# Performance work log

Measured on AMD Instinct MI355X. Metric: run time of the kernel, lower is better.

Reference implementation:

```python
import jax, jax.numpy as jnp
import numpy as np

B, N, D, H = 2, 2048, 1024, 16
HD = D // H  # head_dim = 64
LN_EPS = 1e-5


def rotate_half(x):
    # x: [..., HD] with interleaved pairs -> (-x2, x1) interleaved back
    x = x.reshape(*x.shape[:-1], HD // 2, 2)
    x1, x2 = x[..., 0], x[..., 1]
    return jnp.stack((-x2, x1), axis=-1).reshape(*x.shape[:-2], HD)


def setup_inputs() -> dict:
    key = jax.random.key(0)
    ks = jax.random.split(key, 12)
    s = 0.02
    return {
        "descriptor": jax.random.normal(ks[0], (B, N, D), dtype=jnp.float32),
        "encoding": jax.random.normal(ks[1], (2, B, H, N, HD), dtype=jnp.float32),
        "w_qkv": s * jax.random.normal(ks[2], (3 * D, D), dtype=jnp.float32),
        "b_qkv": jnp.zeros((3 * D,), dtype=jnp.float32),
        "w_out": s * jax.random.normal(ks[3], (D, D), dtype=jnp.float32),
        "b_out": jnp.zeros((D,), dtype=jnp.float32),
        "w_ffn1": s * jax.random.normal(ks[4], (2 * D, 2 * D), dtype=jnp.float32),
        "b_ffn1": jnp.zeros((2 * D,), dtype=jnp.float32),
        "ln_g": jnp.ones((2 * D,), dtype=jnp.float32),
        "ln_b": jnp.zeros((2 * D,), dtype=jnp.float32),
        "w_ffn2": s * jax.random.normal(ks[5], (D, 2 * D), dtype=jnp.float32),
        "b_ffn2": jnp.zeros((D,), dtype=jnp.float32),
    }


def reference(descriptor, encoding, w_qkv, b_qkv, w_out, b_out,
              w_ffn1, b_ffn1, ln_g, ln_b, w_ffn2, b_ffn2):
    # fused QKV projection; last dim laid out as (H, HD, 3) like the torch code
    qkv = descriptor @ w_qkv.T + b_qkv                      # [B, N, 3D]
    qkv = qkv.reshape(B, N, H, HD, 3).transpose(0, 2, 1, 3, 4)  # [B, H, N, HD, 3]
    q, k, v = qkv[..., 0], qkv[..., 1], qkv[..., 2]

    # cached rotary embedding
    q = q * encoding[0] + rotate_half(q) * encoding[1]
    k = k * encoding[0] + rotate_half(k) * encoding[1]

    # scaled dot-product attention (no mask)
    scale = 1.0 / jnp.sqrt(jnp.asarray(HD, dtype=q.dtype))
    scores = jnp.einsum('bhqd,bhkd->bhqk', q, k) * scale    # [B, H, N, N]
    attn = jax.nn.softmax(scores, axis=-1)
    context = jnp.einsum('bhqk,bhkd->bhqd', attn, v)        # [B, H, N, HD]

    message = context.transpose(0, 2, 1, 3).reshape(B, N, D) @ w_out.T + b_out

    # concat-FFN: Linear -> LayerNorm -> GELU -> Linear
    h = jnp.concatenate([descriptor, message], axis=-1) @ w_ffn1.T + b_ffn1  # [B, N, 2D]
    mu = jnp.mean(h, axis=-1, keepdims=True)
    var = jnp.mean(jnp.square(h - mu), axis=-1, keepdims=True)
    h = (h - mu) * jax.lax.rsqrt(var + LN_EPS) * ln_g + ln_b
    h = jax.nn.gelu(h, approximate=False)
    return descriptor + h @ w_ffn2.T + b_ffn2
```

## Files before the change

kernel.cpp:

```cpp
#include <hip/hip_runtime.h>
#include <hip/hip_bf16.h>
#include <stdint.h>
#include <stddef.h>

#define B_   2
#define N_   2048
#define D_   1024
#define H_   16
#define HD_  64
#define BH_  (B_ * H_)
#define M_   (B_ * N_)

typedef short bf16x8 __attribute__((ext_vector_type(8)));
typedef float f32x4  __attribute__((ext_vector_type(4)));

static __device__ __forceinline__ unsigned short f2bf(float f) {
    union { float f; unsigned u; } c; c.f = f;
    unsigned r = (c.u + 0x7FFFu + ((c.u >> 16) & 1u)) >> 16;
    return (unsigned short)r;
}
static __device__ __forceinline__ float bf2f(unsigned short u) {
    union { unsigned u; float f; } c; c.u = ((unsigned)u) << 16; return c.f;
}

#define GLDS16(g, l)                                                                     \
    __builtin_amdgcn_global_load_lds((const __attribute__((address_space(1))) void*)(g), \
                                     (__attribute__((address_space(3))) void*)(l), 16, 0, 0)

__global__ __launch_bounds__(256) void k_cast(const float* __restrict__ in,
                                              unsigned short* __restrict__ out, int n) {
    int i = (blockIdx.x * 256 + threadIdx.x) * 4;
    if (i >= n) return;
    float4 v = *(const float4*)(in + i);
    ushort4 o;
    o.x = f2bf(v.x); o.y = f2bf(v.y); o.z = f2bf(v.z); o.w = f2bf(v.w);
    *(ushort4*)(out + i) = o;
}

__global__ __launch_bounds__(256) void k_cast_desc(const float* __restrict__ in,
                                                   unsigned short* __restrict__ cat) {
    int i = (blockIdx.x * 256 + threadIdx.x) * 4;
    float4 v = *(const float4*)(in + i);
    int row = i >> 10, col = i & 1023;
    ushort4 o;
    o.x = f2bf(v.x); o.y = f2bf(v.y); o.z = f2bf(v.z); o.w = f2bf(v.w);
    *(ushort4*)(cat + (size_t)row * 2048 + col) = o;
}

template <int EPI>
__global__ __launch_bounds__(256) void k_gemm(const unsigned short* __restrict__ A, int lda,
                                              const unsigned short* __restrict__ Bm, int ldb,
                                              void* __restrict__ Cv, int ldc,
                                              const float* __restrict__ bias,
                                              const float* __restrict__ resid, int ldr,
                                              unsigned short* __restrict__ qd,
                                              unsigned short* __restrict__ kd,
                                              unsigned short* __restrict__ vd,
                                              int K) {
    __shared__ unsigned short As[128 * 64];
    __shared__ unsigned short Bs[128 * 64];
    const int tid  = threadIdx.x;
    const int wave = tid >> 6, lane = tid & 63;
    const int wr = wave >> 1, wc = wave & 1;
    const int brow = blockIdx.y * 128, bcol = blockIdx.x * 128;

    const int srow = (lane >> 3);
    const int scol = (lane & 7) * 8;
    const int frow = lane & 15;
    const int fk   = (lane >> 4) * 8;

    f32x4 acc[4][4] = {};

    for (int kt = 0; kt < K; kt += 64) {
        __syncthreads();
#pragma unroll
        for (int j = 0; j < 4; ++j) {
            int r = wave * 32 + j * 8 + srow;
            GLDS16(A  + (size_t)(brow + r) * lda + kt + scol, (char*)As + wave * 4096 + j * 1024);
            GLDS16(Bm + (size_t)(bcol + r) * ldb + kt + scol, (char*)Bs + wave * 4096 + j * 1024);
        }
        __syncthreads();
#pragma unroll
        for (int ks = 0; ks < 2; ++ks) {
            bf16x8 a[4], b[4];
#pragma unroll
            for (int m = 0; m < 4; ++m)
                a[m] = *(const bf16x8*)(As + (wr * 64 + m * 16 + frow) * 64 + ks * 32 + fk);
#pragma unroll
            for (int n = 0; n < 4; ++n)
                b[n] = *(const bf16x8*)(Bs + (wc * 64 + n * 16 + frow) * 64 + ks * 32 + fk);
#pragma unroll
            for (int m = 0; m < 4; ++m)
#pragma unroll
                for (int n = 0; n < 4; ++n)
                    acc[m][n] = __builtin_amdgcn_mfma_f32_16x16x32_bf16(a[m], b[n], acc[m][n], 0, 0, 0);
        }
    }

    const int orow = (lane >> 4) * 4;
#pragma unroll
    for (int m = 0; m < 4; ++m) {
        int row0 = brow + wr * 64 + m * 16 + orow;
#pragma unroll
        for (int n = 0; n < 4; ++n) {
            int col = bcol + wc * 64 + n * 16 + frow;
            float bs = bias[col];
#pragma unroll
            for (int r = 0; r < 4; ++r) {
                float v = acc[m][n][r] + bs;
                if (EPI == 3) {
                    int row = row0 + r;
                    int bb = row >> 11, nr = row & (N_ - 1);
                    int h = col / 192;
                    int rem = col - h * 192;
                    int d = rem / 3;
                    int c = rem - d * 3;
                    unsigned short* dst = (c == 0) ? qd : (c == 1) ? kd : vd;
                    dst[(((size_t)(bb * H_ + h)) * N_ + nr) * 64 + d] = f2bf(v);
                } else if (EPI == 2) {
                    v += resid[(size_t)(row0 + r) * ldr + col];
                    ((float*)Cv)[(size_t)(row0 + r) * ldc + col] = v;
                } else {
                    ((unsigned short*)Cv)[(size_t)(row0 + r) * ldc + col] = f2bf(v);
                }
            }
        }
    }
}

__global__ __launch_bounds__(256) void k_rope_ip(unsigned short* __restrict__ Qb,
                                                 unsigned short* __restrict__ Kb,
                                                 const float* __restrict__ enc) {
    int idx = blockIdx.x * 256 + threadIdx.x;
    int i  = idx & 31;
    int n  = (idx >> 5) & (N_ - 1);
    int bh = idx >> 16;
    size_t eoff = ((size_t)bh * N_ + n) * 64 + i * 2;
    float2 e0 = *(const float2*)(enc + eoff);
    float2 e1 = *(const float2*)(enc + (size_t)BH_ * N_ * 64 + eoff);
    ushort2 qp = *(const ushort2*)(Qb + eoff);
    ushort2 kp = *(const ushort2*)(Kb + eoff);
    float q1 = bf2f(qp.x), q2 = bf2f(qp.y);
    float k1 = bf2f(kp.x), k2 = bf2f(kp.y);
    ushort2 qo, ko;
    qo.x = f2bf(q1 * e0.x - q2 * e1.x);
    qo.y = f2bf(q2 * e0.y + q1 * e1.y);
    ko.x = f2bf(k1 * e0.x - k2 * e1.x);
    ko.y = f2bf(k2 * e0.y + k1 * e1.y);
    *(ushort2*)(Qb + eoff) = qo;
    *(ushort2*)(Kb + eoff) = ko;
}

__global__ __launch_bounds__(256) void k_transpose_v(const unsigned short* __restrict__ Vb,
                                                     unsigned short* __restrict__ Vt) {
    __shared__ unsigned short t[64][72];
    int bh = blockIdx.y, n0 = blockIdx.x * 64;
    int tid = threadIdx.x;
    int r  = tid >> 2;
    int c0 = (tid & 3) * 16;
    const unsigned short* src = Vb + ((size_t)bh * N_ + n0 + r) * 64 + c0;
    *(bf16x8*)(&t[r][c0])     = *(const bf16x8*)(src);
    *(bf16x8*)(&t[r][c0 + 8]) = *(const bf16x8*)(src + 8);
    __syncthreads();
    int d  = tid >> 2;
    int nc = (tid & 3) * 16;
    bf16x8 o0, o1;
#pragma unroll
    for (int j = 0; j < 8; ++j) { o0[j] = (short)t[nc + j][d]; o1[j] = (short)t[nc + 8 + j][d]; }
    unsigned short* dst = Vt + ((size_t)bh * 64 + d) * N_ + n0 + nc;
    *(bf16x8*)(dst)     = o0;
    *(bf16x8*)(dst + 8) = o1;
}

__global__ __launch_bounds__(256) void k_attn(const unsigned short* __restrict__ Qb,
                                              const unsigned short* __restrict__ Kb,
                                              const unsigned short* __restrict__ Vt,
                                              unsigned short* __restrict__ Ctx) {
    __shared__ unsigned short Ks[64 * 64];
    __shared__ unsigned short Vs[64 * 64];
    __shared__ unsigned short Ps[4][16 * 64];
    int bh = blockIdx.y;
    int b = bh >> 4, h = bh & 15;
    int q0 = blockIdx.x * 64;
    int tid = threadIdx.x, wave = tid >> 6, lane = tid & 63;
    int frow = lane & 15, fk = (lane >> 4) * 8, g = lane >> 4;

    const unsigned short* qptr = Qb + ((size_t)bh * N_ + q0 + wave * 16 + frow) * 64;
    bf16x8 qf[2];
    qf[0] = *(const bf16x8*)(qptr + fk);
    qf[1] = *(const bf16x8*)(qptr + 32 + fk);

    float mrow[4] = {-INFINITY, -INFINITY, -INFINITY, -INFINITY};
    float lrow[4] = {0.f, 0.f, 0.f, 0.f};
    f32x4 accO[4] = {};

    for (int kt = 0; kt < N_; kt += 64) {
        __syncthreads();
#pragma unroll
        for (int j = 0; j < 2; ++j) {
            int r = wave * 16 + j * 8 + (lane >> 3);
            GLDS16(Kb + ((size_t)bh * N_ + kt + r) * 64 + (lane & 7) * 8,
                   (char*)Ks + wave * 2048 + j * 1024);
            GLDS16(Vt + ((size_t)bh * 64 + r) * N_ + kt + (lane & 7) * 8,
                   (char*)Vs + wave * 2048 + j * 1024);
        }
        __syncthreads();

        f32x4 s[4];
#pragma unroll
        for (int kc = 0; kc < 4; ++kc) {
            f32x4 a = {};
#pragma unroll
            for (int ks = 0; ks < 2; ++ks) {
                bf16x8 kfr = *(const bf16x8*)(Ks + (kc * 16 + frow) * 64 + ks * 32 + fk);
                a = __builtin_amdgcn_mfma_f32_16x16x32_bf16(qf[ks], kfr, a, 0, 0, 0);
            }
            s[kc] = a * 0.125f;
        }

        float scl[4];
#pragma unroll
        for (int r = 0; r < 4; ++r) {
            float mx = fmaxf(fmaxf(s[0][r], s[1][r]), fmaxf(s[2][r], s[3][r]));
            mx = fmaxf(mx, __shfl_xor(mx, 1));
            mx = fmaxf(mx, __shfl_xor(mx, 2));
            mx = fmaxf(mx, __shfl_xor(mx, 4));
            mx = fmaxf(mx, __shfl_xor(mx, 8));
            float mn = fmaxf(mrow[r], mx);
            float sc = __expf(mrow[r] - mn);
            mrow[r] = mn;
            float ps = 0.f;
#pragma unroll
            for (int kc = 0; kc < 4; ++kc) {
                float p = __expf(s[kc][r] - mn);
                s[kc][r] = p;
                ps += p;
            }
            ps += __shfl_xor(ps, 1);
            ps += __shfl_xor(ps, 2);
            ps += __shfl_xor(ps, 4);
            ps += __shfl_xor(ps, 8);
            lrow[r] = lrow[r] * sc + ps;
            scl[r] = sc;
        }
#pragma unroll
        for (int df = 0; df < 4; ++df)
#pragma unroll
            for (int r = 0; r < 4; ++r) accO[df][r] *= scl[r];

#pragma unroll
        for (int kc = 0; kc < 4; ++kc)
#pragma unroll
            for (int r = 0; r < 4; ++r)
                Ps[wave][(g * 4 + r) * 64 + kc * 16 + frow] = f2bf(s[kc][r]);
        asm volatile("s_waitcnt lgkmcnt(0)" ::: "memory");
        __builtin_amdgcn_sched_barrier(0);

#pragma unroll
        for (int ks = 0; ks < 2; ++ks) {
            bf16x8 pa = *(const bf16x8*)(&Ps[wave][frow * 64 + ks * 32 + fk]);
#pragma unroll
            for (int df = 0; df < 4; ++df) {
                bf16x8 vf = *(const bf16x8*)(Vs + (df * 16 + frow) * 64 + ks * 32 + fk);
                accO[df] = __builtin_amdgcn_mfma_f32_16x16x32_bf16(pa, vf, accO[df], 0, 0, 0);
            }
        }
    }

#pragma unroll
    for (int df = 0; df < 4; ++df)
#pragma unroll
        for (int r = 0; r < 4; ++r) {
            int q = q0 + wave * 16 + g * 4 + r;
            float v = accO[df][r] / lrow[r];
            Ctx[((size_t)(b * N_ + q)) * D_ + h * 64 + df * 16 + frow] = f2bf(v);
        }
}

__global__ __launch_bounds__(256) void k_ln_gelu(const unsigned short* __restrict__ hsrc,
                                                 const float* __restrict__ gma,
                                                 const float* __restrict__ bta,
                                                 unsigned short* __restrict__ out) {
    __shared__ float red[2][4];
    int row = blockIdx.x, tid = threadIdx.x;
    const unsigned short* hr = hsrc + (size_t)row * 2048 + tid * 8;
    bf16x8 hv = *(const bf16x8*)(hr);
    float xs[8];
    float s = 0.f, q = 0.f;
#pragma unroll
    for (int j = 0; j < 8; ++j) {
        float x = bf2f((unsigned short)hv[j]);
        xs[j] = x; s += x; q += x * x;
    }
#pragma unroll
    for (int off = 1; off < 64; off <<= 1) {
        s += __shfl_xor(s, off);
        q += __shfl_xor(q, off);
    }
    int wave = tid >> 6;
    if ((tid & 63) == 0) { red[0][wave] = s; red[1][wave] = q; }
    __syncthreads();
    s = red[0][0] + red[0][1] + red[0][2] + red[0][3];
    q = red[1][0] + red[1][1] + red[1][2] + red[1][3];
    float mu   = s * (1.f / 2048.f);
    float var  = q * (1.f / 2048.f) - mu * mu;
    float rstd = rsqrtf(var + 1e-5f);
    int c = tid * 8;
#pragma unroll
    for (int j = 0; j < 8; ++j) {
        float x = (xs[j] - mu) * rstd * gma[c + j] + bta[c + j];
        float y = 0.5f * x * (1.f + erff(x * 0.70710678118654752f));
        out[(size_t)row * 2048 + c + j] = f2bf(y);
    }
}

extern "C" void kernel_launch(void* const* d_in, const int* in_sizes, int n_in,
                              void* d_out, int out_size, void* d_ws, size_t ws_size,
                              hipStream_t stream) {
    const float* descriptor = (const float*)d_in[0];
    const float* encoding   = (const float*)d_in[1];
    const float* w_qkv      = (const float*)d_in[2];
    const float* b_qkv      = (const float*)d_in[3];
    const float* w_out      = (const float*)d_in[4];
    const float* b_out      = (const float*)d_in[5];
    const float* w_ffn1     = (const float*)d_in[6];
    const float* b_ffn1     = (const float*)d_in[7];
    const float* ln_g       = (const float*)d_in[8];
    const float* ln_b       = (const float*)d_in[9];
    const float* w_ffn2     = (const float*)d_in[10];
    const float* b_ffn2     = (const float*)d_in[11];
    float* out = (float*)d_out;

    char* ws = (char*)d_ws;
    unsigned short* wffn1_b = (unsigned short*)(ws);
    unsigned short* wffn2_b = (unsigned short*)(ws + ((size_t)8  << 20));
    unsigned short* wout_b  = (unsigned short*)(ws + ((size_t)12 << 20));
    unsigned short* cat     = (unsigned short*)(ws + ((size_t)14 << 20));
    unsigned short* Qb      = (unsigned short*)(ws + ((size_t)30 << 20));
    unsigned short* Kb      = (unsigned short*)(ws + ((size_t)38 << 20));
    unsigned short* Vb      = (unsigned short*)(ws + ((size_t)46 << 20));
    unsigned short* wqkv_b  = (unsigned short*)(ws + ((size_t)54 << 20));
    unsigned short* Vt      = (unsigned short*)(ws + ((size_t)54 << 20));
    unsigned short* msg     = (unsigned short*)(ws + ((size_t)46 << 20));
    unsigned short* hbuf    = (unsigned short*)(ws + ((size_t)30 << 20));
    unsigned short* h2      = (unsigned short*)(ws + ((size_t)14 << 20));

    k_cast_desc<<<4096, 256, 0, stream>>>(descriptor, cat);
    k_cast<<<3072, 256, 0, stream>>>(w_qkv, wqkv_b, 3145728);
    k_cast<<<1024, 256, 0, stream>>>(w_out, wout_b, 1048576);
    k_cast<<<4096, 256, 0, stream>>>(w_ffn1, wffn1_b, 4194304);
    k_cast<<<2048, 256, 0, stream>>>(w_ffn2, wffn2_b, 2097152);

    k_gemm<3><<<dim3(24, 32), 256, 0, stream>>>(cat, 2048, wqkv_b, 1024, nullptr, 0,
                                                b_qkv, nullptr, 0, Qb, Kb, Vb, 1024);
    k_rope_ip<<<8192, 256, 0, stream>>>(Qb, Kb, encoding);
    k_transpose_v<<<dim3(32, 32), 256, 0, stream>>>(Vb, Vt);
    k_attn<<<dim3(32, 32), 256, 0, stream>>>(Qb, Kb, Vt, msg);
    k_gemm<1><<<dim3(8, 32), 256, 0, stream>>>(msg, 1024, wout_b, 1024, cat + 1024, 2048,
                                               b_out, nullptr, 0, nullptr, nullptr, nullptr, 1024);
    k_gemm<1><<<dim3(16, 32), 256, 0, stream>>>(cat, 2048, wffn1_b, 2048, hbuf, 2048,
                                                b_ffn1, nullptr, 0, nullptr, nullptr, nullptr, 2048);
    k_ln_gelu<<<4096, 256, 0, stream>>>(hbuf, ln_g, ln_b, h2);
    k_gemm<2><<<dim3(8, 32), 256, 0, stream>>>(h2, 2048, wffn2_b, 2048, out, 1024,
                                               b_ffn2, descriptor, 1024, nullptr, nullptr, nullptr, 2048);
}
```

Baseline: 521.5 us.

## Double-buffer attention K/V tiles, swizzle LDS, fold scale into exp2, merge weight casts

The attention kernel now double-buffers its K/V tiles in LDS, prefetching the next tile while computing the current one, which removes one barrier per iteration. LDS reads and writes use an XOR swizzle to avoid bank conflicts. The softmax scale times log2(e) is folded into Q during RoPE so the kernel can use exp2f and skip the per-score multiply. The change also adds wave priority hints, remaps blocks across heads, uses a reciprocal for the final normalization, and merges the four weight cast launches into one. Together these raise LDS usage and mix several unrelated changes.

```diff
diff --git a/kernel.cpp b/kernel.cpp
--- a/kernel.cpp
+++ b/kernel.cpp
@@ -27,14 +27,26 @@
     __builtin_amdgcn_global_load_lds((const __attribute__((address_space(1))) void*)(g), \
                                      (__attribute__((address_space(3))) void*)(l), 16, 0, 0)
 
-__global__ __launch_bounds__(256) void k_cast(const float* __restrict__ in,
-                                              unsigned short* __restrict__ out, int n) {
-    int i = (blockIdx.x * 256 + threadIdx.x) * 4;
-    if (i >= n) return;
-    float4 v = *(const float4*)(in + i);
+#define QSCALE 0.18033688011112042f
+
+__global__ __launch_bounds__(256) void k_cast_w4(const float* __restrict__ s0,
+                                                 const float* __restrict__ s1,
+                                                 const float* __restrict__ s2,
+                                                 const float* __restrict__ s3,
+                                                 unsigned short* __restrict__ d0,
+                                                 unsigned short* __restrict__ d1,
+                                                 unsigned short* __restrict__ d2,
+                                                 unsigned short* __restrict__ d3) {
+    int i = blockIdx.x * 256 + threadIdx.x;
+    const float* s; unsigned short* d; int off;
+    if (i < 786432)              { s = s0; d = d0; off = i; }
+    else if (i < 1048576)        { s = s1; d = d1; off = i - 786432; }
+    else if (i < 2097152)        { s = s2; d = d2; off = i - 1048576; }
+    else                         { s = s3; d = d3; off = i - 2097152; }
+    float4 v = *(const float4*)(s + (size_t)off * 4);
     ushort4 o;
     o.x = f2bf(v.x); o.y = f2bf(v.y); o.z = f2bf(v.z); o.w = f2bf(v.w);
-    *(ushort4*)(out + i) = o;
+    *(ushort4*)(d + (size_t)off * 4) = o;
 }
 
 __global__ __launch_bounds__(256) void k_cast_desc(const float* __restrict__ in,
@@ -143,8 +155,8 @@
     float q1 = bf2f(qp.x), q2 = bf2f(qp.y);
     float k1 = bf2f(kp.x), k2 = bf2f(kp.y);
     ushort2 qo, ko;
-    qo.x = f2bf(q1 * e0.x - q2 * e1.x);
-    qo.y = f2bf(q2 * e0.y + q1 * e1.y);
+    qo.x = f2bf((q1 * e0.x - q2 * e1.x) * QSCALE);
+    qo.y = f2bf((q2 * e0.y + q1 * e1.y) * QSCALE);
     ko.x = f2bf(k1 * e0.x - k2 * e1.x);
     ko.y = f2bf(k2 * e0.y + k1 * e1.y);
     *(ushort2*)(Qb + eoff) = qo;
@@ -176,14 +188,36 @@
                                               const unsigned short* __restrict__ Kb,
                                               const unsigned short* __restrict__ Vt,
                                               unsigned short* __restrict__ Ctx) {
-    __shared__ unsigned short Ks[64 * 64];
-    __shared__ unsigned short Vs[64 * 64];
+    __shared__ unsigned short Ks[2][64 * 64];
+    __shared__ unsigned short Vs[2][64 * 64];
     __shared__ unsigned short Ps[4][16 * 64];
-    int bh = blockIdx.y;
+
+    int lin = blockIdx.x + 32 * blockIdx.y;
+    int ixc = lin >> 3;
+    int bh  = (lin & 7) * 4 + (ixc >> 5);
+    int q0  = (ixc & 31) * 64;
     int b = bh >> 4, h = bh & 15;
-    int q0 = blockIdx.x * 64;
     int tid = threadIdx.x, wave = tid >> 6, lane = tid & 63;
     int frow = lane & 15, fk = (lane >> 4) * 8, g = lane >> 4;
+    int f7x8 = (frow & 7) * 8;
+
+    int srow = lane >> 3;
+    int scol = ((lane & 7) ^ srow) * 8;
+
+    const unsigned short* Kbh = Kb + (size_t)bh * N_ * 64;
+    const unsigned short* Vbh = Vt + (size_t)bh * 64 * N_;
+
+#define ATTN_STAGE(bufi, kt)                                                           \
+    do {                                                                               \
+        _Pragma("unroll")                                                              \
+        for (int j = 0; j < 2; ++j) {                                                  \
+            int rr = wave * 16 + j * 8 + srow;                                         \
+            GLDS16(Kbh + (size_t)((kt) + rr) * 64 + scol,                              \
+                   (char*)Ks[bufi] + wave * 2048 + j * 1024);                          \
+            GLDS16(Vbh + (size_t)rr * N_ + (kt) + scol,                                \
+                   (char*)Vs[bufi] + wave * 2048 + j * 1024);                          \
+        }                                                                              \
+    } while (0)
 
     const unsigned short* qptr = Qb + ((size_t)bh * N_ + q0 + wave * 16 + frow) * 64;
     bf16x8 qf[2];
@@ -194,29 +228,26 @@
     float lrow[4] = {0.f, 0.f, 0.f, 0.f};
     f32x4 accO[4] = {};
 
-    for (int kt = 0; kt < N_; kt += 64) {
+    ATTN_STAGE(0, 0);
+
+    for (int t = 0; t < N_ / 64; ++t) {
+        int cur = t & 1;
         __syncthreads();
-#pragma unroll
-        for (int j = 0; j < 2; ++j) {
-            int r = wave * 16 + j * 8 + (lane >> 3);
-            GLDS16(Kb + ((size_t)bh * N_ + kt + r) * 64 + (lane & 7) * 8,
-                   (char*)Ks + wave * 2048 + j * 1024);
-            GLDS16(Vt + ((size_t)bh * 64 + r) * N_ + kt + (lane & 7) * 8,
-                   (char*)Vs + wave * 2048 + j * 1024);
-        }
-        __syncthreads();
+        if (t + 1 < N_ / 64) ATTN_STAGE(cur ^ 1, (t + 1) * 64);
 
         f32x4 s[4];
+        __builtin_amdgcn_s_setprio(1);
 #pragma unroll
         for (int kc = 0; kc < 4; ++kc) {
             f32x4 a = {};
 #pragma unroll
             for (int ks = 0; ks < 2; ++ks) {
-                bf16x8 kfr = *(const bf16x8*)(Ks + (kc * 16 + frow) * 64 + ks * 32 + fk);
+                bf16x8 kfr = *(const bf16x8*)(Ks[cur] + (kc * 16 + frow) * 64 + ((ks * 32 + fk) ^ f7x8));
                 a = __builtin_amdgcn_mfma_f32_16x16x32_bf16(qf[ks], kfr, a, 0, 0, 0);
             }
-            s[kc] = a * 0.125f;
-        }
+            s[kc] = a;
+        }
+        __builtin_amdgcn_s_setprio(0);
 
         float scl[4];
 #pragma unroll
@@ -227,12 +258,12 @@
             mx = fmaxf(mx, __shfl_xor(mx, 4));
             mx = fmaxf(mx, __shfl_xor(mx, 8));
             float mn = fmaxf(mrow[r], mx);
-            float sc = __expf(mrow[r] - mn);
+            float sc = exp2f(mrow[r] - mn);
             mrow[r] = mn;
             float ps = 0.f;
 #pragma unroll
             for (int kc = 0; kc < 4; ++kc) {
-                float p = __expf(s[kc][r] - mn);
+                float p = exp2f(s[kc][r] - mn);
                 s[kc][r] = p;
                 ps += p;
             }
@@ -251,30 +282,37 @@
 #pragma unroll
         for (int kc = 0; kc < 4; ++kc)
 #pragma unroll
-            for (int r = 0; r < 4; ++r)
-                Ps[wave][(g * 4 + r) * 64 + kc * 16 + frow] = f2bf(s[kc][r]);
+            for (int r = 0; r < 4; ++r) {
+                int prow = g * 4 + r;
+                Ps[wave][prow * 64 + ((kc * 16 + frow) ^ ((prow & 7) * 8))] = f2bf(s[kc][r]);
+            }
         asm volatile("s_waitcnt lgkmcnt(0)" ::: "memory");
         __builtin_amdgcn_sched_barrier(0);
 
+        __builtin_amdgcn_s_setprio(1);
 #pragma unroll
         for (int ks = 0; ks < 2; ++ks) {
-            bf16x8 pa = *(const bf16x8*)(&Ps[wave][frow * 64 + ks * 32 + fk]);
+            bf16x8 pa = *(const bf16x8*)(&Ps[wave][frow * 64 + ((ks * 32 + fk) ^ f7x8)]);
 #pragma unroll
             for (int df = 0; df < 4; ++df) {
-                bf16x8 vf = *(const bf16x8*)(Vs + (df * 16 + frow) * 64 + ks * 32 + fk);
+                bf16x8 vf = *(const bf16x8*)(Vs[cur] + (df * 16 + frow) * 64 + ((ks * 32 + fk) ^ f7x8));
                 accO[df] = __builtin_amdgcn_mfma_f32_16x16x32_bf16(pa, vf, accO[df], 0, 0, 0);
             }
         }
-    }
-
+        __builtin_amdgcn_s_setprio(0);
+    }
+
+    float inv[4];
+#pragma unroll
+    for (int r = 0; r < 4; ++r) inv[r] = 1.0f / lrow[r];
 #pragma unroll
     for (int df = 0; df < 4; ++df)
 #pragma unroll
         for (int r = 0; r < 4; ++r) {
             int q = q0 + wave * 16 + g * 4 + r;
-            float v = accO[df][r] / lrow[r];
-            Ctx[((size_t)(b * N_ + q)) * D_ + h * 64 + df * 16 + frow] = f2bf(v);
-        }
+            Ctx[((size_t)(b * N_ + q)) * D_ + h * 64 + df * 16 + frow] = f2bf(accO[df][r] * inv[r]);
+        }
+#undef ATTN_STAGE
 }
 
 __global__ __launch_bounds__(256) void k_ln_gelu(const unsigned short* __restrict__ hsrc,
@@ -346,10 +384,8 @@
     unsigned short* h2      = (unsigned short*)(ws + ((size_t)14 << 20));
 
     k_cast_desc<<<4096, 256, 0, stream>>>(descriptor, cat);
-    k_cast<<<3072, 256, 0, stream>>>(w_qkv, wqkv_b, 3145728);
-    k_cast<<<1024, 256, 0, stream>>>(w_out, wout_b, 1048576);
-    k_cast<<<4096, 256, 0, stream>>>(w_ffn1, wffn1_b, 4194304);
-    k_cast<<<2048, 256, 0, stream>>>(w_ffn2, wffn2_b, 2097152);
+    k_cast_w4<<<10240, 256, 0, stream>>>(w_qkv, w_out, w_ffn1, w_ffn2,
+                                         wqkv_b, wout_b, wffn1_b, wffn2_b);
 
     k_gemm<3><<<dim3(24, 32), 256, 0, stream>>>(cat, 2048, wqkv_b, 1024, nullptr, 0,
                                                 b_qkv, nullptr, 0, Qb, Kb, Vb, 1024);
```

Result: faster. 482.1 us (-7.6%).
